# Kernel tuning notes

Hardware: AMD Instinct MI355X
Metric: run time of the kernel (lower is better)

The kernel has to match this reference:

```python
import math
import jax, jax.numpy as jnp
import numpy as np

IN_DIM, OUT_DIM = 256, 128
IN_SEQ, OUT_SEQ = 512, 512
NUM_BASIS = 16
LN_EPS = 1e-5
TWO_PI = 2.0 * math.pi


def _make_periods():
    # periods[i, j, g] = i*(out_dim*num_basis) + j*num_basis + g + 2
    i = np.arange(OUT_DIM)[:, None, None]
    j = np.arange(OUT_DIM)[None, :, None]
    g = np.arange(NUM_BASIS)[None, None, :]
    return jnp.asarray((i * (OUT_DIM * NUM_BASIS) + j * NUM_BASIS + g + 2).astype(np.float32))


def setup_inputs() -> dict:
    key = jax.random.key(0)
    kx, kM, kP, kL = jax.random.split(key, 4)
    x = jax.random.normal(kx, (IN_SEQ, IN_DIM), dtype=jnp.float32)
    M = jax.random.normal(kM, (OUT_DIM, IN_DIM), dtype=jnp.float32) * 0.5
    P = jax.random.normal(kP, (OUT_DIM, OUT_DIM, NUM_BASIS), dtype=jnp.float32) * 0.1
    Linker = jax.random.normal(kL, (IN_SEQ, OUT_SEQ), dtype=jnp.float32) * 0.1
    gamma = jnp.ones((OUT_DIM,), dtype=jnp.float32)
    beta = jnp.zeros((OUT_DIM,), dtype=jnp.float32)
    periods = _make_periods()  # (O, O, B) constant buffer
    return {"x": x, "M": M, "P": P, "Linker": Linker,
            "gamma": gamma, "beta": beta, "periods": periods}


def reference(x, M, P, Linker, gamma, beta, periods):
    # Projection: Z = x @ M.T  -> (S, O)
    Z = x @ M.T
    # LayerNorm over last dim
    mu = jnp.mean(Z, axis=-1, keepdims=True)
    var = jnp.mean(jnp.square(Z - mu), axis=-1, keepdims=True)
    Zn = (Z - mu) * jax.lax.rsqrt(var + LN_EPS) * gamma + beta
    # Position transform: T[k,i] = sum_{j,g} Zn[k,j] * P[i,j,g] * cos(2*pi*k / periods[i,j,g])
    k = jnp.arange(Z.shape[0], dtype=jnp.float32)[:, None, None, None]  # (S,1,1,1)
    phi = jnp.cos(TWO_PI * k / periods)  # (S, O, O, B)
    T = jnp.einsum('kj,ijg,kijg->ki', Zn, P, phi)  # (S, O)
    # Sequence transform: U = Linker.T @ T -> (out_seq, O)
    U = Linker.T @ T
    # 'shared' residual uses pre-LayerNorm projection x @ M.T
    residual = Linker.T @ Z
    return U + residual
```

## Files before the change

### kernel.cpp

```cpp
#include <hip/hip_runtime.h>

#define IN_DIM   256
#define OUT_DIM  128
#define IN_SEQ   512
#define OUT_SEQ  512
#define NUM_BASIS 16
#define LN_EPS   1e-5f
#define KC       64

__device__ __forceinline__ float cosrev(float x) {
  return __builtin_amdgcn_cosf(__builtin_amdgcn_fractf(x));
}

__global__ __launch_bounds__(256) void kA(const float* __restrict__ x,
                                          const float* __restrict__ M,
                                          const float* __restrict__ gamma,
                                          const float* __restrict__ beta,
                                          float* __restrict__ Zn,
                                          float* __restrict__ ZT) {
  const int k = blockIdx.x;
  const int t = threadIdx.x;
  __shared__ __align__(16) float xk[IN_DIM];
  __shared__ float red[256];
  __shared__ float stats[8];

  xk[t] = x[k * IN_DIM + t];
  __syncthreads();

  const int j = t & 127;
  const int h = t >> 7;
  const float4* __restrict__ M4 = reinterpret_cast<const float4*>(M + j * IN_DIM + h * 128);
  const float4* __restrict__ x4 = reinterpret_cast<const float4*>(xk + h * 128);
  float acc = 0.f;
#pragma unroll 8
  for (int c = 0; c < 32; ++c) {
    float4 m = M4[c];
    float4 xv = x4[c];
    acc = fmaf(m.x, xv.x, acc);
    acc = fmaf(m.y, xv.y, acc);
    acc = fmaf(m.z, xv.z, acc);
    acc = fmaf(m.w, xv.w, acc);
  }
  red[t] = acc;
  __syncthreads();

  float z = 0.f;
  if (t < 128) z = red[t] + red[t + 128];

  float s1 = (t < 128) ? z : 0.f;
  float s2 = (t < 128) ? z * z : 0.f;
#pragma unroll
  for (int m = 1; m < 64; m <<= 1) {
    s1 += __shfl_xor(s1, m);
    s2 += __shfl_xor(s2, m);
  }
  const int w = t >> 6;
  if ((t & 63) == 0) {
    stats[w] = s1;
    stats[4 + w] = s2;
  }
  __syncthreads();
  const float mu  = (stats[0] + stats[1] + stats[2] + stats[3]) * (1.f / 128.f);
  const float msq = (stats[4] + stats[5] + stats[6] + stats[7]) * (1.f / 128.f);
  const float rs  = rsqrtf(msq - mu * mu + LN_EPS);

  if (t < 128) {
    float zn = (z - mu) * rs * gamma[t] + beta[t];
    Zn[k * OUT_DIM + t] = zn;
    ZT[t * IN_SEQ + k] = z;
  }
}

__global__ __launch_bounds__(128) void kB(const float* __restrict__ P,
                                          const float* __restrict__ Zn,
                                          const float* __restrict__ ZT,
                                          float* __restrict__ V) {
  const int i  = blockIdx.y;
  const int k0 = blockIdx.x * KC;
  const int j  = threadIdx.x;
  const int w  = j >> 6;

  __shared__ float red[KC * 2];

  float Pv[NUM_BASIS], tc[NUM_BASIS], c0[NUM_BASIS], c1[NUM_BASIS];
  {
    const float4* __restrict__ P4 =
        reinterpret_cast<const float4*>(P + (size_t)(i * OUT_DIM + j) * NUM_BASIS);
    float4 pl[4] = {P4[0], P4[1], P4[2], P4[3]};
#pragma unroll
    for (int q = 0; q < 4; ++q) {
      Pv[4 * q + 0] = pl[q].x;
      Pv[4 * q + 1] = pl[q].y;
      Pv[4 * q + 2] = pl[q].z;
      Pv[4 * q + 3] = pl[q].w;
    }
  }
  const int pb = i * (OUT_DIM * NUM_BASIS) + j * NUM_BASIS + 2;
  const float km1 = (float)(k0 - 1);
  const float kcu = (float)k0;
#pragma unroll
  for (int g = 0; g < NUM_BASIS; ++g) {
    float pinv = 1.0f / (float)(pb + g);
    tc[g] = 2.0f * __builtin_amdgcn_cosf(pinv);
    c0[g] = cosrev(km1 * pinv);
    c1[g] = cosrev(kcu * pinv);
  }

  const float* __restrict__ znj = Zn + j;
  float buf[4];
#pragma unroll
  for (int r = 0; r < 4; ++r) buf[r] = znj[(k0 + r) * OUT_DIM];

  for (int kg = 0; kg < KC / 4; ++kg) {
    float nbuf[4];
#pragma unroll
    for (int r = 0; r < 4; ++r) {
      nbuf[r] = znj[(k0 + (kg + 1) * 4 + r) * OUT_DIM];
    }
#pragma unroll
    for (int r = 0; r < 4; ++r) {
      float s = 0.f;
#pragma unroll
      for (int g = 0; g < NUM_BASIS; ++g) s = fmaf(Pv[g], c1[g], s);
      float v = buf[r] * s;
#pragma unroll
      for (int m = 1; m < 64; m <<= 1) v += __shfl_xor(v, m);
      if ((j & 63) == 0) red[(kg * 4 + r) * 2 + w] = v;
#pragma unroll
      for (int g = 0; g < NUM_BASIS; ++g) {
        float cn = fmaf(tc[g], c1[g], -c0[g]);
        c0[g] = c1[g];
        c1[g] = cn;
      }
    }
#pragma unroll
    for (int r = 0; r < 4; ++r) buf[r] = nbuf[r];
  }

  __syncthreads();
  if (j < KC) {
    const int k = k0 + j;
    V[k * OUT_DIM + i] = red[j * 2] + red[j * 2 + 1] + ZT[i * IN_SEQ + k];
  }
}

__global__ __launch_bounds__(512) void kC(const float* __restrict__ L,
                                          const float* __restrict__ V,
                                          float* __restrict__ out) {
  const int s = blockIdx.x;
  const int t = threadIdx.x;
  const int i = t & 127;
  const int q = t >> 7;
  __shared__ float Lcol[IN_SEQ];
  __shared__ float red[4 * OUT_DIM];

  Lcol[t] = L[t * OUT_SEQ + s];
  __syncthreads();

  const int k0 = q * 128;
  float acc = 0.f;
#pragma unroll 8
  for (int kk = 0; kk < 128; ++kk) {
    const int k = k0 + kk;
    acc = fmaf(Lcol[k], V[k * OUT_DIM + i], acc);
  }
  red[q * OUT_DIM + i] = acc;
  __syncthreads();

  if (t < OUT_DIM) {
    out[s * OUT_DIM + t] =
        red[t] + red[OUT_DIM + t] + red[2 * OUT_DIM + t] + red[3 * OUT_DIM + t];
  }
}

extern "C" void kernel_launch(void* const* d_in, const int* in_sizes, int n_in,
                              void* d_out, int out_size, void* d_ws, size_t ws_size,
                              hipStream_t stream) {
  const float* x      = (const float*)d_in[0];
  const float* M      = (const float*)d_in[1];
  const float* P      = (const float*)d_in[2];
  const float* Linker = (const float*)d_in[3];
  const float* gamma  = (const float*)d_in[4];
  const float* beta   = (const float*)d_in[5];
  float* out = (float*)d_out;

  float* ws = (float*)d_ws;
  float* Zn = ws;
  float* ZT = ws + IN_SEQ * OUT_DIM;
  float* V  = ws + 2 * IN_SEQ * OUT_DIM;

  kA<<<dim3(IN_SEQ), dim3(256), 0, stream>>>(x, M, gamma, beta, Zn, ZT);
  kB<<<dim3(IN_SEQ / KC, OUT_DIM), dim3(128), 0, stream>>>(P, Zn, ZT, V);
  kC<<<dim3(OUT_SEQ), dim3(512), 0, stream>>>(Linker, V, out);
}
```

Baseline: 43.32 us.

## Fuse three kernels into one cooperative kernel with grid-wide syncs

Replaces the three separate launches (projection+LayerNorm, cosine position transform, Linker matmul) with one cooperative kernel of 512 blocks that separates the stages with grid.sync(). The stage-B work is remapped so each block handles one output column and 128 sequence rows across two half-blocks, and the shuffle reductions are batched over 8 rows. The aim is to remove launch gaps between kernels. In exchange it pays the cost of grid barriers, needs all 512 blocks co-resident, and gives the final matmul stage half as many threads per row.

```diff
diff --git a/kernel.cpp b/kernel.cpp
--- a/kernel.cpp
+++ b/kernel.cpp
@@ -1,4 +1,7 @@
 #include <hip/hip_runtime.h>
+#include <hip/hip_cooperative_groups.h>
+
+namespace cg = cooperative_groups;
 
 #define IN_DIM   256
 #define OUT_DIM  128
@@ -6,170 +9,180 @@
 #define OUT_SEQ  512
 #define NUM_BASIS 16
 #define LN_EPS   1e-5f
-#define KC       64
 
 __device__ __forceinline__ float cosrev(float x) {
   return __builtin_amdgcn_cosf(__builtin_amdgcn_fractf(x));
 }
 
-__global__ __launch_bounds__(256) void kA(const float* __restrict__ x,
-                                          const float* __restrict__ M,
-                                          const float* __restrict__ gamma,
-                                          const float* __restrict__ beta,
-                                          float* __restrict__ Zn,
-                                          float* __restrict__ ZT) {
-  const int k = blockIdx.x;
+__global__ __launch_bounds__(256, 2) void fused(
+    const float* __restrict__ x, const float* __restrict__ M,
+    const float* __restrict__ P, const float* __restrict__ L,
+    const float* __restrict__ gamma, const float* __restrict__ beta,
+    float* __restrict__ Zn, float* __restrict__ ZT,
+    float* __restrict__ V, float* __restrict__ out) {
+  cg::grid_group grid = cg::this_grid();
+  const int b = blockIdx.x;
   const int t = threadIdx.x;
+
   __shared__ __align__(16) float xk[IN_DIM];
-  __shared__ float red[256];
+  __shared__ float redA[256];
   __shared__ float stats[8];
-
-  xk[t] = x[k * IN_DIM + t];
-  __syncthreads();
-
-  const int j = t & 127;
-  const int h = t >> 7;
-  const float4* __restrict__ M4 = reinterpret_cast<const float4*>(M + j * IN_DIM + h * 128);
-  const float4* __restrict__ x4 = reinterpret_cast<const float4*>(xk + h * 128);
-  float acc = 0.f;
+  __shared__ float redB[128 * 2];
+  __shared__ float Lcol[IN_SEQ];
+  __shared__ float redC[2 * OUT_DIM];
+
+  {
+    const int k = b;
+    xk[t] = x[k * IN_DIM + t];
+    __syncthreads();
+
+    const int j = t & 127;
+    const int h = t >> 7;
+    const float4* __restrict__ M4 =
+        reinterpret_cast<const float4*>(M + j * IN_DIM + h * 128);
+    const float4* __restrict__ x4 = reinterpret_cast<const float4*>(xk + h * 128);
+    float acc = 0.f;
 #pragma unroll 8
-  for (int c = 0; c < 32; ++c) {
-    float4 m = M4[c];
-    float4 xv = x4[c];
-    acc = fmaf(m.x, xv.x, acc);
-    acc = fmaf(m.y, xv.y, acc);
-    acc = fmaf(m.z, xv.z, acc);
-    acc = fmaf(m.w, xv.w, acc);
+    for (int c = 0; c < 32; ++c) {
+      float4 m = M4[c];
+      float4 xv = x4[c];
+      acc = fmaf(m.x, xv.x, acc);
+      acc = fmaf(m.y, xv.y, acc);
+      acc = fmaf(m.z, xv.z, acc);
+      acc = fmaf(m.w, xv.w, acc);
+    }
+    redA[t] = acc;
+    __syncthreads();
+
+    float z = 0.f;
+    if (t < 128) z = redA[t] + redA[t + 128];
+
+    float s1 = (t < 128) ? z : 0.f;
+    float s2 = (t < 128) ? z * z : 0.f;
+#pragma unroll
+    for (int m = 1; m < 64; m <<= 1) {
+      s1 += __shfl_xor(s1, m);
+      s2 += __shfl_xor(s2, m);
+    }
+    const int w = t >> 6;
+    if ((t & 63) == 0) {
+      stats[w] = s1;
+      stats[4 + w] = s2;
+    }
+    __syncthreads();
+    const float mu  = (stats[0] + stats[1] + stats[2] + stats[3]) * (1.f / 128.f);
+    const float msq = (stats[4] + stats[5] + stats[6] + stats[7]) * (1.f / 128.f);
+    const float rs  = rsqrtf(msq - mu * mu + LN_EPS);
+
+    if (t < 128) {
+      float zn = (z - mu) * rs * gamma[t] + beta[t];
+      Zn[k * OUT_DIM + t] = zn;
+      ZT[t * IN_SEQ + k] = z;
+    }
   }
-  red[t] = acc;
-  __syncthreads();
-
-  float z = 0.f;
-  if (t < 128) z = red[t] + red[t + 128];
-
-  float s1 = (t < 128) ? z : 0.f;
-  float s2 = (t < 128) ? z * z : 0.f;
-#pragma unroll
-  for (int m = 1; m < 64; m <<= 1) {
-    s1 += __shfl_xor(s1, m);
-    s2 += __shfl_xor(s2, m);
+
+  grid.sync();
+
+  {
+    const int i     = b & 127;
+    const int chunk = b >> 7;
+    const int j     = t & 127;
+    const int kh    = t >> 7;
+    const int w01   = (t >> 6) & 1;
+    const int ks0   = chunk * 128 + kh * 64;
+
+    float Pv[NUM_BASIS], tc[NUM_BASIS], c0[NUM_BASIS], c1[NUM_BASIS];
+    {
+      const float4* __restrict__ P4 =
+          reinterpret_cast<const float4*>(P + (size_t)(i * OUT_DIM + j) * NUM_BASIS);
+      float4 pl[4] = {P4[0], P4[1], P4[2], P4[3]};
+#pragma unroll
+      for (int q = 0; q < 4; ++q) {
+        Pv[4 * q + 0] = pl[q].x;
+        Pv[4 * q + 1] = pl[q].y;
+        Pv[4 * q + 2] = pl[q].z;
+        Pv[4 * q + 3] = pl[q].w;
+      }
+    }
+    const int pb = i * (OUT_DIM * NUM_BASIS) + j * NUM_BASIS + 2;
+    const float km1 = (float)(ks0 - 1);
+    const float kcu = (float)ks0;
+#pragma unroll
+    for (int g = 0; g < NUM_BASIS; ++g) {
+      float pinv = 1.0f / (float)(pb + g);
+      tc[g] = 2.0f * __builtin_amdgcn_cosf(pinv);
+      c0[g] = cosrev(km1 * pinv);
+      c1[g] = cosrev(kcu * pinv);
+    }
+
+    const float* __restrict__ znj = Zn + j;
+    float buf[8];
+#pragma unroll
+    for (int r = 0; r < 8; ++r) buf[r] = znj[(ks0 + r) * OUT_DIM];
+
+    for (int kg = 0; kg < 8; ++kg) {
+      float nbuf[8];
+#pragma unroll
+      for (int r = 0; r < 8; ++r) {
+        nbuf[r] = znj[(ks0 + (kg + 1) * 8 + r) * OUT_DIM];
+      }
+      float v[8];
+#pragma unroll
+      for (int r = 0; r < 8; ++r) {
+        float s = 0.f;
+#pragma unroll
+        for (int g = 0; g < NUM_BASIS; ++g) s = fmaf(Pv[g], c1[g], s);
+        v[r] = buf[r] * s;
+#pragma unroll
+        for (int g = 0; g < NUM_BASIS; ++g) {
+          float cn = fmaf(tc[g], c1[g], -c0[g]);
+          c0[g] = c1[g];
+          c1[g] = cn;
+        }
+      }
+#pragma unroll
+      for (int m = 1; m < 64; m <<= 1) {
+#pragma unroll
+        for (int r = 0; r < 8; ++r) v[r] += __shfl_xor(v[r], m);
+      }
+      if ((t & 63) == 0) {
+#pragma unroll
+        for (int r = 0; r < 8; ++r) redB[(kh * 64 + kg * 8 + r) * 2 + w01] = v[r];
+      }
+#pragma unroll
+      for (int r = 0; r < 8; ++r) buf[r] = nbuf[r];
+    }
+
+    __syncthreads();
+    if (t < 128) {
+      const int k = chunk * 128 + t;
+      V[k * OUT_DIM + i] = redB[t * 2] + redB[t * 2 + 1] + ZT[i * IN_SEQ + k];
+    }
   }
-  const int w = t >> 6;
-  if ((t & 63) == 0) {
-    stats[w] = s1;
-    stats[4 + w] = s2;
-  }
-  __syncthreads();
-  const float mu  = (stats[0] + stats[1] + stats[2] + stats[3]) * (1.f / 128.f);
-  const float msq = (stats[4] + stats[5] + stats[6] + stats[7]) * (1.f / 128.f);
-  const float rs  = rsqrtf(msq - mu * mu + LN_EPS);
-
-  if (t < 128) {
-    float zn = (z - mu) * rs * gamma[t] + beta[t];
-    Zn[k * OUT_DIM + t] = zn;
-    ZT[t * IN_SEQ + k] = z;
-  }
-}
-
-__global__ __launch_bounds__(128) void kB(const float* __restrict__ P,
-                                          const float* __restrict__ Zn,
-                                          const float* __restrict__ ZT,
-                                          float* __restrict__ V) {
-  const int i  = blockIdx.y;
-  const int k0 = blockIdx.x * KC;
-  const int j  = threadIdx.x;
-  const int w  = j >> 6;
-
-  __shared__ float red[KC * 2];
-
-  float Pv[NUM_BASIS], tc[NUM_BASIS], c0[NUM_BASIS], c1[NUM_BASIS];
+
+  grid.sync();
+
   {
-    const float4* __restrict__ P4 =
-        reinterpret_cast<const float4*>(P + (size_t)(i * OUT_DIM + j) * NUM_BASIS);
-    float4 pl[4] = {P4[0], P4[1], P4[2], P4[3]};
-#pragma unroll
-    for (int q = 0; q < 4; ++q) {
-      Pv[4 * q + 0] = pl[q].x;
-      Pv[4 * q + 1] = pl[q].y;
-      Pv[4 * q + 2] = pl[q].z;
-      Pv[4 * q + 3] = pl[q].w;
-    }
-  }
-  const int pb = i * (OUT_DIM * NUM_BASIS) + j * NUM_BASIS + 2;
-  const float km1 = (float)(k0 - 1);
-  const float kcu = (float)k0;
-#pragma unroll
-  for (int g = 0; g < NUM_BASIS; ++g) {
-    float pinv = 1.0f / (float)(pb + g);
-    tc[g] = 2.0f * __builtin_amdgcn_cosf(pinv);
-    c0[g] = cosrev(km1 * pinv);
-    c1[g] = cosrev(kcu * pinv);
-  }
-
-  const float* __restrict__ znj = Zn + j;
-  float buf[4];
-#pragma unroll
-  for (int r = 0; r < 4; ++r) buf[r] = znj[(k0 + r) * OUT_DIM];
-
-  for (int kg = 0; kg < KC / 4; ++kg) {
-    float nbuf[4];
-#pragma unroll
-    for (int r = 0; r < 4; ++r) {
-      nbuf[r] = znj[(k0 + (kg + 1) * 4 + r) * OUT_DIM];
-    }
-#pragma unroll
-    for (int r = 0; r < 4; ++r) {
-      float s = 0.f;
-#pragma unroll
-      for (int g = 0; g < NUM_BASIS; ++g) s = fmaf(Pv[g], c1[g], s);
-      float v = buf[r] * s;
-#pragma unroll
-      for (int m = 1; m < 64; m <<= 1) v += __shfl_xor(v, m);
-      if ((j & 63) == 0) red[(kg * 4 + r) * 2 + w] = v;
-#pragma unroll
-      for (int g = 0; g < NUM_BASIS; ++g) {
-        float cn = fmaf(tc[g], c1[g], -c0[g]);
-        c0[g] = c1[g];
-        c1[g] = cn;
-      }
-    }
-#pragma unroll
-    for (int r = 0; r < 4; ++r) buf[r] = nbuf[r];
-  }
-
-  __syncthreads();
-  if (j < KC) {
-    const int k = k0 + j;
-    V[k * OUT_DIM + i] = red[j * 2] + red[j * 2 + 1] + ZT[i * IN_SEQ + k];
-  }
-}
-
-__global__ __launch_bounds__(512) void kC(const float* __restrict__ L,
-                                          const float* __restrict__ V,
-                                          float* __restrict__ out) {
-  const int s = blockIdx.x;
-  const int t = threadIdx.x;
-  const int i = t & 127;
-  const int q = t >> 7;
-  __shared__ float Lcol[IN_SEQ];
-  __shared__ float red[4 * OUT_DIM];
-
-  Lcol[t] = L[t * OUT_SEQ + s];
-  __syncthreads();
-
-  const int k0 = q * 128;
-  float acc = 0.f;
+    const int s = b;
+    const int i = t & 127;
+    const int q = t >> 7;
+    Lcol[t] = L[t * OUT_SEQ + s];
+    Lcol[t + 256] = L[(t + 256) * OUT_SEQ + s];
+    __syncthreads();
+
+    const int kb0 = q * 256;
+    float acc = 0.f;
 #pragma unroll 8
-  for (int kk = 0; kk < 128; ++kk) {
-    const int k = k0 + kk;
-    acc = fmaf(Lcol[k], V[k * OUT_DIM + i], acc);
-  }
-  red[q * OUT_DIM + i] = acc;
-  __syncthreads();
-
-  if (t < OUT_DIM) {
-    out[s * OUT_DIM + t] =
-        red[t] + red[OUT_DIM + t] + red[2 * OUT_DIM + t] + red[3 * OUT_DIM + t];
+    for (int kk = 0; kk < 256; ++kk) {
+      const int k = kb0 + kk;
+      acc = fmaf(Lcol[k], V[k * OUT_DIM + i], acc);
+    }
+    redC[q * OUT_DIM + i] = acc;
+    __syncthreads();
+
+    if (t < OUT_DIM) {
+      out[s * OUT_DIM + t] = redC[t] + redC[OUT_DIM + t];
+    }
   }
 }
 
@@ -189,7 +202,9 @@
   float* ZT = ws + IN_SEQ * OUT_DIM;
   float* V  = ws + 2 * IN_SEQ * OUT_DIM;
 
-  kA<<<dim3(IN_SEQ), dim3(256), 0, stream>>>(x, M, gamma, beta, Zn, ZT);
-  kB<<<dim3(IN_SEQ / KC, OUT_DIM), dim3(128), 0, stream>>>(P, Zn, ZT, V);
-  kC<<<dim3(OUT_SEQ), dim3(512), 0, stream>>>(Linker, V, out);
+  void* args[] = {(void*)&x, (void*)&M, (void*)&P, (void*)&Linker,
+                  (void*)&gamma, (void*)&beta, (void*)&Zn, (void*)&ZT,
+                  (void*)&V, (void*)&out};
+  hipLaunchCooperativeKernel(reinterpret_cast<void*>(fused), dim3(512), dim3(256),
+                             args, 0, stream);
 }
```

Result: slower. 152.0 us (+250.8%).
